# Optimization experiments

Measured on AMD Instinct MI355X. Metric: run time of the kernel, lower is better.

## Reference

```python
import jax, jax.numpy as jnp
import numpy as np

D = 32  # embedding_dimension (TGN default memory_dimension == embedding_dimension)


def time_encode(t, w, b):
    # TGN TimeEncode: cos(t * w + b); t: [E] -> [E, D]
    return jnp.cos(t[:, None] * w[None, :] + b[None, :])


def setup_inputs() -> dict:
    key = jax.random.key(0)
    ks = jax.random.split(key, 24)
    N, B, E, F, NE = 1_000_000, 262_144, 1_048_576, 64, 500_000
    inp = {}
    # per-node-type memory tables (Mailbox memory)
    inp["mem_user"] = jax.random.normal(ks[0], (N, D), jnp.float32)
    inp["mem_item"] = jax.random.normal(ks[1], (N, D), jnp.float32)
    # active event node ids per type (memory lookup indices)
    inp["node_ids_user"] = jax.random.randint(ks[2], (B,), 0, N, jnp.int32)
    inp["node_ids_item"] = jax.random.randint(ks[3], (B,), 0, N, jnp.int32)
    # heterogeneous edge lists: user->item and item->user (indices into the B active nodes)
    inp["edge_src_ui"] = jax.random.randint(ks[4], (E,), 0, B, jnp.int32)
    inp["edge_dst_ui"] = jax.random.randint(ks[5], (E,), 0, B, jnp.int32)
    inp["edge_src_iu"] = jax.random.randint(ks[6], (E,), 0, B, jnp.int32)
    inp["edge_dst_iu"] = jax.random.randint(ks[7], (E,), 0, B, jnp.int32)
    inp["edge_idx_ui"] = jax.random.randint(ks[8], (E,), 0, NE, jnp.int32)
    inp["edge_idx_iu"] = jax.random.randint(ks[9], (E,), 0, NE, jnp.int32)
    inp["edge_rel_times_ui"] = jax.random.uniform(ks[10], (E,), jnp.float32) * 1000.0
    inp["edge_rel_times_iu"] = jax.random.uniform(ks[11], (E,), jnp.float32) * 1000.0
    inp["edge_feature"] = jax.random.normal(ks[12], (NE, F), jnp.float32)
    # per-node-type Linear(D, D, bias=False) == self.lin[node_type]
    s = 1.0 / np.sqrt(D)
    inp["W_user"] = jax.random.normal(ks[13], (D, D), jnp.float32) * s
    inp["W_item"] = jax.random.normal(ks[14], (D, D), jnp.float32) * s
    # per-edge-type Linear(F, D) == self.edge_feature_linear[edge_type]
    se = 1.0 / np.sqrt(F)
    inp["We_ui"] = jax.random.normal(ks[15], (F, D), jnp.float32) * se
    inp["be_ui"] = jnp.zeros((D,), jnp.float32)
    inp["We_iu"] = jax.random.normal(ks[16], (F, D), jnp.float32) * se
    inp["be_iu"] = jnp.zeros((D,), jnp.float32)
    # TimeEncode params (standard TGN init: 1/10^linspace)
    inp["time_w"] = jnp.asarray(1.0 / (10.0 ** np.linspace(0, 9, D)), jnp.float32)
    inp["time_b"] = jnp.zeros((D,), jnp.float32)
    # decoder(2*D -> 64 -> 16 -> 1), drop=0
    inp["dec_W1"] = jax.random.normal(ks[17], (2 * D, 64), jnp.float32) * (1.0 / np.sqrt(2 * D))
    inp["dec_b1"] = jnp.zeros((64,), jnp.float32)
    inp["dec_W2"] = jax.random.normal(ks[18], (64, 16), jnp.float32) * 0.125
    inp["dec_b2"] = jnp.zeros((16,), jnp.float32)
    inp["dec_W3"] = jax.random.normal(ks[19], (16, 1), jnp.float32) * 0.25
    inp["dec_b3"] = jnp.zeros((1,), jnp.float32)
    return inp


def reference(mem_user, mem_item, edge_feature, edge_rel_times_ui, edge_rel_times_iu,
              W_user, W_item, We_ui, be_ui, We_iu, be_iu, time_w, time_b,
              dec_W1, dec_b1, dec_W2, dec_b2, dec_W3, dec_b3,
              node_ids_user, node_ids_item, edge_src_ui, edge_dst_ui,
              edge_src_iu, edge_dst_iu, edge_idx_ui, edge_idx_iu):
    B = node_ids_user.shape[0]
    # memory lookup + per-node-type linear (self.lin[node_type], bias=False)
    h_user = mem_user[node_ids_user] @ W_user   # [B, D]
    h_item = mem_item[node_ids_item] @ W_item   # [B, D]
    # heterogeneous message passing: src memory + edge-feature linear + time encoding,
    # scattered (segment_sum) onto destination nodes per edge type
    msg_ui = (h_user[edge_src_ui]
              + edge_feature[edge_idx_ui] @ We_ui + be_ui
              + time_encode(edge_rel_times_ui, time_w, time_b))  # [E, D]
    agg_item = jax.ops.segment_sum(msg_ui, edge_dst_ui, num_segments=B)
    msg_iu = (h_item[edge_src_iu]
              + edge_feature[edge_idx_iu] @ We_iu + be_iu
              + time_encode(edge_rel_times_iu, time_w, time_b))  # [E, D]
    agg_user = jax.ops.segment_sum(msg_iu, edge_dst_iu, num_segments=B)
    hu = jax.nn.relu(h_user + agg_user)
    hi = jax.nn.relu(h_item + agg_item)
    # decoder `distance` on concatenated pair embeddings (2*D -> 64 -> 16 -> 1), drop=0
    z = jnp.concatenate([hu, hi], axis=-1)      # [B, 2D]
    x = jax.nn.relu(z @ dec_W1 + dec_b1)
    x = jax.nn.relu(x @ dec_W2 + dec_b2)
    return x @ dec_W3 + dec_b3                   # [B, 1]
```

## Files before the change

### kernel.cpp

```cpp
#include <hip/hip_runtime.h>

#define DEV __device__ __forceinline__

DEV unsigned short f2bf(float x) {
    unsigned u = __float_as_uint(x);
    unsigned r = (u + 0x7FFFu + ((u >> 16) & 1u)) >> 16;
    return (unsigned short)r;
}
DEV unsigned pack_bf2(float a, float b) {
    return (unsigned)f2bf(a) | ((unsigned)f2bf(b) << 16);
}
DEV float bf2f(unsigned short v) {
    return __uint_as_float(((unsigned)v) << 16);
}
DEV float fastcos(float x) {
    float r = x * 0.15915494309189535f;
    r = r - floorf(r);
    return __builtin_amdgcn_cosf(r);
}

__global__ void prep_kernel(const float* __restrict__ W_user, const float* __restrict__ W_item,
                            const float* __restrict__ We_ui, const float* __restrict__ be_ui,
                            const float* __restrict__ We_iu, const float* __restrict__ be_iu,
                            const float* __restrict__ dW1, const float* __restrict__ dW2,
                            float* __restrict__ Wt_user, float* __restrict__ Wt_item,
                            float* __restrict__ Wct, float* __restrict__ bc,
                            float* __restrict__ W1t, float* __restrict__ W2t) {
    int t = threadIdx.x;
    for (int i = t; i < 1024; i += 256) {
        int k = i / 32, d = i % 32;
        Wt_user[d * 32 + k] = W_user[i];
        Wt_item[d * 32 + k] = W_item[i];
    }
    for (int i = t; i < 4096; i += 256) {
        int j = i / 64, k = i % 64;
        Wct[i] = (j < 32) ? We_ui[k * 32 + j] : We_iu[k * 32 + (j - 32)];
    }
    for (int i = t; i < 64; i += 256)
        bc[i] = (i < 32) ? be_ui[i] : be_iu[i - 32];
    for (int i = t; i < 4096; i += 256) {
        int j = i / 64, k = i % 64;
        W1t[i] = dW1[k * 64 + j];
    }
    for (int i = t; i < 1024; i += 256) {
        int c = i / 64, j = i % 64;
        W2t[i] = dW2[j * 16 + c];
    }
}

__global__ __launch_bounds__(256) void node_linear_kernel(
        const float* __restrict__ mem, const int* __restrict__ ids,
        const float* __restrict__ Wt, float* __restrict__ h, int B) {
    int r = blockIdx.x * 256 + threadIdx.x;
    if (r >= B) return;
    int id = ids[r];
    const float4* m4 = (const float4*)(mem + (size_t)id * 32);
    float m[32];
#pragma unroll
    for (int q = 0; q < 8; ++q) {
        float4 v = m4[q];
        m[4 * q + 0] = v.x; m[4 * q + 1] = v.y; m[4 * q + 2] = v.z; m[4 * q + 3] = v.w;
    }
    float* hr = h + (size_t)r * 32;
    for (int db = 0; db < 8; ++db) {
        float acc[4];
#pragma unroll
        for (int u = 0; u < 4; ++u) {
            const float* wr = Wt + (size_t)(db * 4 + u) * 32;
            float a = 0.f;
#pragma unroll
            for (int k = 0; k < 32; ++k) a = fmaf(m[k], wr[k], a);
            acc[u] = a;
        }
        float4 o; o.x = acc[0]; o.y = acc[1]; o.z = acc[2]; o.w = acc[3];
        *(float4*)(hr + db * 4) = o;
    }
}

__global__ __launch_bounds__(256) void proj_kernel(
        const float* __restrict__ feat, const float* __restrict__ Wct,
        const float* __restrict__ bc, unsigned short* __restrict__ proj, int NE) {
    int r = blockIdx.x * 256 + threadIdx.x;
    if (r >= NE) return;
    const float4* f4 = (const float4*)(feat + (size_t)r * 64);
    float f[64];
#pragma unroll
    for (int q = 0; q < 16; ++q) {
        float4 v = f4[q];
        f[4 * q + 0] = v.x; f[4 * q + 1] = v.y; f[4 * q + 2] = v.z; f[4 * q + 3] = v.w;
    }
    unsigned short* orow = proj + (size_t)r * 64;
    for (int jb = 0; jb < 8; ++jb) {
        float acc[8];
#pragma unroll
        for (int u = 0; u < 8; ++u) acc[u] = bc[jb * 8 + u];
#pragma unroll
        for (int u = 0; u < 8; ++u) {
            const float* wr = Wct + (size_t)(jb * 8 + u) * 64;
#pragma unroll
            for (int k = 0; k < 64; ++k) acc[u] = fmaf(f[k], wr[k], acc[u]);
        }
        uint4 p;
        p.x = pack_bf2(acc[0], acc[1]);
        p.y = pack_bf2(acc[2], acc[3]);
        p.z = pack_bf2(acc[4], acc[5]);
        p.w = pack_bf2(acc[6], acc[7]);
        *(uint4*)(orow + jb * 8) = p;
    }
}

__global__ __launch_bounds__(256) void edge_kernel(
        const int* __restrict__ src, const int* __restrict__ dst,
        const int* __restrict__ eidx, const float* __restrict__ rt,
        const float* __restrict__ h, const unsigned short* __restrict__ proj,
        float* __restrict__ agg,
        const float* __restrict__ tw, const float* __restrict__ tb, int E) {
    long long i = (long long)blockIdx.x * 256 + threadIdx.x;
    int e = (int)(i >> 5), d = (int)(i & 31);
    if (e >= E) return;
    int s = src[e], dd = dst[e], ix = eidx[e];
    float t = rt[e];
    float c = fastcos(fmaf(t, tw[d], tb[d]));
    float pv = bf2f(proj[(size_t)ix * 64 + d]);
    float m = h[(size_t)s * 32 + d] + pv + c;
    unsafeAtomicAdd(&agg[(size_t)dd * 32 + d], m);
}

__global__ __launch_bounds__(256) void decoder_kernel(
        const float* __restrict__ h_user, const float* __restrict__ h_item,
        const float* __restrict__ agg_user, const float* __restrict__ agg_item,
        const float* __restrict__ W1t, const float* __restrict__ b1,
        const float* __restrict__ W2t, const float* __restrict__ b2,
        const float* __restrict__ W3, const float* __restrict__ b3,
        float* __restrict__ out, int B) {
    int i = blockIdx.x * 256 + threadIdx.x;
    if (i >= B) return;
    float z[64];
    {
        const float4* a4 = (const float4*)(h_user + (size_t)i * 32);
        const float4* b4 = (const float4*)(agg_user + (size_t)i * 32);
#pragma unroll
        for (int q = 0; q < 8; ++q) {
            float4 a = a4[q], b = b4[q];
            z[4 * q + 0] = fmaxf(a.x + b.x, 0.f);
            z[4 * q + 1] = fmaxf(a.y + b.y, 0.f);
            z[4 * q + 2] = fmaxf(a.z + b.z, 0.f);
            z[4 * q + 3] = fmaxf(a.w + b.w, 0.f);
        }
    }
    {
        const float4* a4 = (const float4*)(h_item + (size_t)i * 32);
        const float4* b4 = (const float4*)(agg_item + (size_t)i * 32);
#pragma unroll
        for (int q = 0; q < 8; ++q) {
            float4 a = a4[q], b = b4[q];
            z[32 + 4 * q + 0] = fmaxf(a.x + b.x, 0.f);
            z[32 + 4 * q + 1] = fmaxf(a.y + b.y, 0.f);
            z[32 + 4 * q + 2] = fmaxf(a.z + b.z, 0.f);
            z[32 + 4 * q + 3] = fmaxf(a.w + b.w, 0.f);
        }
    }
    float x2[16];
#pragma unroll
    for (int c = 0; c < 16; ++c) x2[c] = b2[c];
    for (int jb = 0; jb < 8; ++jb) {
        float a[8];
#pragma unroll
        for (int u = 0; u < 8; ++u) {
            int j = jb * 8 + u;
            const float* wr = W1t + (size_t)j * 64;
            float acc = b1[j];
#pragma unroll
            for (int k = 0; k < 64; ++k) acc = fmaf(z[k], wr[k], acc);
            a[u] = fmaxf(acc, 0.f);
        }
#pragma unroll
        for (int c = 0; c < 16; ++c) {
            const float* w2r = W2t + (size_t)c * 64 + jb * 8;
            float acc = x2[c];
#pragma unroll
            for (int u = 0; u < 8; ++u) acc = fmaf(a[u], w2r[u], acc);
            x2[c] = acc;
        }
    }
    float o = b3[0];
#pragma unroll
    for (int c = 0; c < 16; ++c) o = fmaf(fmaxf(x2[c], 0.f), W3[c], o);
    out[i] = o;
}

extern "C" void kernel_launch(void* const* d_in, const int* in_sizes, int n_in,
                              void* d_out, int out_size, void* d_ws, size_t ws_size,
                              hipStream_t stream) {
    const float* mem_user = (const float*)d_in[0];
    const float* mem_item = (const float*)d_in[1];
    const int*   ids_user = (const int*)d_in[2];
    const int*   ids_item = (const int*)d_in[3];
    const int*   src_ui   = (const int*)d_in[4];
    const int*   dst_ui   = (const int*)d_in[5];
    const int*   src_iu   = (const int*)d_in[6];
    const int*   dst_iu   = (const int*)d_in[7];
    const int*   eidx_ui  = (const int*)d_in[8];
    const int*   eidx_iu  = (const int*)d_in[9];
    const float* rt_ui    = (const float*)d_in[10];
    const float* rt_iu    = (const float*)d_in[11];
    const float* feat     = (const float*)d_in[12];
    const float* W_user   = (const float*)d_in[13];
    const float* W_item   = (const float*)d_in[14];
    const float* We_ui    = (const float*)d_in[15];
    const float* be_ui    = (const float*)d_in[16];
    const float* We_iu    = (const float*)d_in[17];
    const float* be_iu    = (const float*)d_in[18];
    const float* tw       = (const float*)d_in[19];
    const float* tb       = (const float*)d_in[20];
    const float* dW1      = (const float*)d_in[21];
    const float* db1      = (const float*)d_in[22];
    const float* dW2      = (const float*)d_in[23];
    const float* db2      = (const float*)d_in[24];
    const float* dW3      = (const float*)d_in[25];
    const float* db3      = (const float*)d_in[26];

    const int B  = in_sizes[2];
    const int E  = in_sizes[4];
    const int NE = in_sizes[12] / 64;

    float* w = (float*)d_ws;
    const size_t hsz = (size_t)B * 32;
    float* h_user   = w;
    float* h_item   = h_user + hsz;
    float* agg_user = h_item + hsz;
    float* agg_item = agg_user + hsz;
    float* Wt_user  = agg_item + hsz;
    float* Wt_item  = Wt_user + 1024;
    float* Wct      = Wt_item + 1024;
    float* bc       = Wct + 4096;
    float* W1t      = bc + 64;
    float* W2t      = W1t + 4096;
    unsigned short* proj = (unsigned short*)(W2t + 1024);

    prep_kernel<<<1, 256, 0, stream>>>(W_user, W_item, We_ui, be_ui, We_iu, be_iu, dW1, dW2,
                                       Wt_user, Wt_item, Wct, bc, W1t, W2t);
    node_linear_kernel<<<(B + 255) / 256, 256, 0, stream>>>(mem_user, ids_user, Wt_user, h_user, B);
    node_linear_kernel<<<(B + 255) / 256, 256, 0, stream>>>(mem_item, ids_item, Wt_item, h_item, B);
    hipMemsetAsync(agg_user, 0, 2 * hsz * sizeof(float), stream);
    proj_kernel<<<(NE + 255) / 256, 256, 0, stream>>>(feat, Wct, bc, proj, NE);

    long long tot = (long long)E * 32;
    int eblocks = (int)((tot + 255) / 256);
    edge_kernel<<<eblocks, 256, 0, stream>>>(src_ui, dst_ui, eidx_ui, rt_ui,
                                             h_user, proj + 0, agg_item, tw, tb, E);
    edge_kernel<<<eblocks, 256, 0, stream>>>(src_iu, dst_iu, eidx_iu, rt_iu,
                                             h_item, proj + 32, agg_user, tw, tb, E);
    decoder_kernel<<<(B + 255) / 256, 256, 0, stream>>>(h_user, h_item, agg_user, agg_item,
                                                        W1t, db1, W2t, db2, dW3, db3,
                                                        (float*)d_out, B);
}
```

Measured before the change: 885.2 us.

## Compute edge-feature projection with bf16 MFMA instead of scalar FMAs

Replaces the per-thread scalar fp32 projection of the 500K×64 edge-feature table onto both edge-type weights with a wave-level 32x32x16 bf16 MFMA kernel. Weights are pre-packed into MFMA fragment layout in the prep kernel, and inputs are converted to bf16 on load. Results are staged through LDS so each row is written to global memory with coalesced stores. The scalar version had a heavy compute loop of 64×64 FMAs per row, but the inputs are now rounded to bf16, which lowers precision.

```diff
diff --git a/kernel.cpp b/kernel.cpp
--- a/kernel.cpp
+++ b/kernel.cpp
@@ -1,6 +1,9 @@
 #include <hip/hip_runtime.h>
 
 #define DEV __device__ __forceinline__
+
+typedef __attribute__((ext_vector_type(8))) short short8;
+typedef __attribute__((ext_vector_type(16))) float float16;
 
 DEV unsigned short f2bf(float x) {
     unsigned u = __float_as_uint(x);
@@ -24,7 +27,7 @@
                             const float* __restrict__ We_iu, const float* __restrict__ be_iu,
                             const float* __restrict__ dW1, const float* __restrict__ dW2,
                             float* __restrict__ Wt_user, float* __restrict__ Wt_item,
-                            float* __restrict__ Wct, float* __restrict__ bc,
+                            unsigned short* __restrict__ Wb, float* __restrict__ bc,
                             float* __restrict__ W1t, float* __restrict__ W2t) {
     int t = threadIdx.x;
     for (int i = t; i < 1024; i += 256) {
@@ -33,8 +36,16 @@
         Wt_item[d * 32 + k] = W_item[i];
     }
     for (int i = t; i < 4096; i += 256) {
-        int j = i / 64, k = i % 64;
-        Wct[i] = (j < 32) ? We_ui[k * 32 + j] : We_iu[k * 32 + (j - 32)];
+        int kt   = i >> 10;
+        int rem  = i & 1023;
+        int n2   = rem >> 9;
+        int rem2 = rem & 511;
+        int l    = rem2 >> 3;
+        int ii   = rem2 & 7;
+        int k = kt * 16 + (l >> 5) * 8 + ii;
+        int n = (l & 31);
+        float v = n2 ? We_iu[k * 32 + n] : We_ui[k * 32 + n];
+        Wb[i] = f2bf(v);
     }
     for (int i = t; i < 64; i += 256)
         bc[i] = (i < 32) ? be_ui[i] : be_iu[i - 32];
@@ -77,35 +88,61 @@
     }
 }
 
-__global__ __launch_bounds__(256) void proj_kernel(
-        const float* __restrict__ feat, const float* __restrict__ Wct,
+__global__ __launch_bounds__(256) void proj_mfma_kernel(
+        const float* __restrict__ feat, const unsigned short* __restrict__ Wb,
         const float* __restrict__ bc, unsigned short* __restrict__ proj, int NE) {
-    int r = blockIdx.x * 256 + threadIdx.x;
-    if (r >= NE) return;
-    const float4* f4 = (const float4*)(feat + (size_t)r * 64);
-    float f[64];
-#pragma unroll
-    for (int q = 0; q < 16; ++q) {
-        float4 v = f4[q];
-        f[4 * q + 0] = v.x; f[4 * q + 1] = v.y; f[4 * q + 2] = v.z; f[4 * q + 3] = v.w;
-    }
-    unsigned short* orow = proj + (size_t)r * 64;
-    for (int jb = 0; jb < 8; ++jb) {
-        float acc[8];
-#pragma unroll
-        for (int u = 0; u < 8; ++u) acc[u] = bc[jb * 8 + u];
-#pragma unroll
-        for (int u = 0; u < 8; ++u) {
-            const float* wr = Wct + (size_t)(jb * 8 + u) * 64;
-#pragma unroll
-            for (int k = 0; k < 64; ++k) acc[u] = fmaf(f[k], wr[k], acc[u]);
-        }
-        uint4 p;
-        p.x = pack_bf2(acc[0], acc[1]);
-        p.y = pack_bf2(acc[2], acc[3]);
-        p.z = pack_bf2(acc[4], acc[5]);
-        p.w = pack_bf2(acc[6], acc[7]);
-        *(uint4*)(orow + jb * 8) = p;
+    __shared__ unsigned short lds[128 * 72];
+    const int lane = threadIdx.x & 63;
+    const int wave = threadIdx.x >> 6;
+    const int col  = lane & 31;
+    const int half = lane >> 5;
+
+    short8 bfrag[8];
+    const short8* wb8 = (const short8*)Wb;
+#pragma unroll
+    for (int f = 0; f < 8; ++f) bfrag[f] = wb8[f * 64 + lane];
+
+    int r = blockIdx.x * 128 + wave * 32 + col;
+    if (r >= NE) r = NE - 1;
+    const float* fr = feat + (size_t)r * 64 + half * 8;
+    short8 afrag[4];
+#pragma unroll
+    for (int t = 0; t < 4; ++t) {
+        float4 a = *(const float4*)(fr + t * 16);
+        float4 b = *(const float4*)(fr + t * 16 + 4);
+        short8 s;
+        s[0] = (short)f2bf(a.x); s[1] = (short)f2bf(a.y);
+        s[2] = (short)f2bf(a.z); s[3] = (short)f2bf(a.w);
+        s[4] = (short)f2bf(b.x); s[5] = (short)f2bf(b.y);
+        s[6] = (short)f2bf(b.z); s[7] = (short)f2bf(b.w);
+        afrag[t] = s;
+    }
+
+    float16 acc0, acc1;
+    float b0 = bc[col], b1 = bc[32 + col];
+#pragma unroll
+    for (int i = 0; i < 16; ++i) { acc0[i] = b0; acc1[i] = b1; }
+#pragma unroll
+    for (int t = 0; t < 4; ++t) {
+        acc0 = __builtin_amdgcn_mfma_f32_32x32x16_bf16(afrag[t], bfrag[t * 2 + 0], acc0, 0, 0, 0);
+        acc1 = __builtin_amdgcn_mfma_f32_32x32x16_bf16(afrag[t], bfrag[t * 2 + 1], acc1, 0, 0, 0);
+    }
+
+#pragma unroll
+    for (int reg = 0; reg < 16; ++reg) {
+        int rl = wave * 32 + (reg & 3) + 8 * (reg >> 2) + 4 * half;
+        lds[rl * 72 + col]      = f2bf(acc0[reg]);
+        lds[rl * 72 + 32 + col] = f2bf(acc1[reg]);
+    }
+    __syncthreads();
+
+    int trow = threadIdx.x >> 1, thalf = threadIdx.x & 1;
+    int grow = blockIdx.x * 128 + trow;
+    if (grow < NE) {
+        const uint4* lsrc = (const uint4*)(lds + trow * 72 + thalf * 32);
+        uint4* gdst = (uint4*)(proj + (size_t)grow * 64 + thalf * 32);
+#pragma unroll
+        for (int s = 0; s < 4; ++s) gdst[s] = lsrc[s];
     }
 }
 
@@ -232,18 +269,18 @@
     float* agg_item = agg_user + hsz;
     float* Wt_user  = agg_item + hsz;
     float* Wt_item  = Wt_user + 1024;
-    float* Wct      = Wt_item + 1024;
-    float* bc       = Wct + 4096;
+    unsigned short* Wb = (unsigned short*)(Wt_item + 1024);
+    float* bc       = (float*)(Wb + 4096);
     float* W1t      = bc + 64;
     float* W2t      = W1t + 4096;
     unsigned short* proj = (unsigned short*)(W2t + 1024);
 
     prep_kernel<<<1, 256, 0, stream>>>(W_user, W_item, We_ui, be_ui, We_iu, be_iu, dW1, dW2,
-                                       Wt_user, Wt_item, Wct, bc, W1t, W2t);
+                                       Wt_user, Wt_item, Wb, bc, W1t, W2t);
     node_linear_kernel<<<(B + 255) / 256, 256, 0, stream>>>(mem_user, ids_user, Wt_user, h_user, B);
     node_linear_kernel<<<(B + 255) / 256, 256, 0, stream>>>(mem_item, ids_item, Wt_item, h_item, B);
     hipMemsetAsync(agg_user, 0, 2 * hsz * sizeof(float), stream);
-    proj_kernel<<<(NE + 255) / 256, 256, 0, stream>>>(feat, Wct, bc, proj, NE);
+    proj_mfma_kernel<<<(NE + 127) / 128, 256, 0, stream>>>(feat, Wb, bc, proj, NE);
 
     long long tot = (long long)E * 32;
     int eblocks = (int)((tot + 255) / 256);
```

New measurement: 801.0 us. 9.5% less time.
